# Performance work log

Hardware: AMD Instinct MI355X
Metric: run time of the kernel (lower is better)

The kernel has to match this reference:

```python
import jax, jax.numpy as jnp
import numpy as np

HEADS = 8

def setup_inputs() -> dict:
    key = jax.random.key(0)
    ks = jax.random.split(key, 6)
    N, C, L = 8, 512, 2048
    s = 0.02
    return {
        'x':  jax.random.normal(ks[0], (N, C, L), dtype=jnp.float32),
        'Wq': jax.random.normal(ks[1], (C, C), dtype=jnp.float32) * s,
        'Wk': jax.random.normal(ks[2], (C, C), dtype=jnp.float32) * s,
        'Wv': jax.random.normal(ks[3], (C, C), dtype=jnp.float32) * s,
        'Wo': jax.random.normal(ks[4], (C, C), dtype=jnp.float32) * s,
        'bo': jnp.zeros((C,), dtype=jnp.float32),
    }

def reference(x, Wq, Wk, Wv, Wo, bo):
    N, C, L = x.shape
    h = HEADS
    d = C // h
    scale = C ** (-0.5)  # note: scales by full channels, as in the original

    def proj(W):
        # Conv1d(k=1, bias=False) == per-position linear: [N,C,L] -> [N,L,h,d]
        y = jnp.einsum('oc,ncl->nlo', W, x)
        return y.reshape(N, L, h, d)

    q, k, v = proj(Wq), proj(Wk), proj(Wv)

    qk = jnp.einsum('nqhd,nkhd->nhqk', q, k)  # [N,h,L,L]
    causal_mask = jnp.tril(jnp.ones((L, L), dtype=bool))
    qk = jnp.where(causal_mask, qk, -jnp.inf)
    attn = jax.nn.softmax(qk * scale, axis=-1)

    out = jnp.einsum('nhqk,nkhd->nqhd', attn, v)  # [N,L,h,d]
    out = out.reshape(N, L, C).transpose(0, 2, 1)  # n (h d) l
    return jnp.einsum('oc,ncl->nol', Wo, out) + bo[None, :, None]
```

## Files before the change

### kernel.cpp

```cpp
#include <hip/hip_runtime.h>
#include <math.h>

typedef __bf16 bf16;
typedef __attribute__((ext_vector_type(8))) __bf16 bf16x8;
typedef __attribute__((ext_vector_type(4))) float f32x4;
typedef unsigned short u16;
typedef unsigned int u32;

constexpr int Nn = 8, Cc = 512, Ll = 2048, Hh = 8, Dd = 64;
constexpr float kScale = 0.044194173824159216f;
constexpr float kQexp2 = kScale * 1.44269504088896341f;
constexpr size_t NCL = (size_t)Nn * Cc * Ll;
constexpr size_t WSZ = (size_t)Cc * Cc;

static __device__ __forceinline__ u16 bfbits(bf16 v) {
    union { bf16 b; u16 u; } x; x.b = v; return x.u;
}
static __device__ __forceinline__ u32 fbits(float f) {
    union { float f; u32 u; } x; x.f = f; return x.u;
}
static __device__ __forceinline__ float fexp2(float x) {
#if __has_builtin(__builtin_amdgcn_exp2f)
    return __builtin_amdgcn_exp2f(x);
#else
    return exp2f(x);
#endif
}

#define MFMA(a, b, c) __builtin_amdgcn_mfma_f32_16x16x32_bf16((a), (b), (c), 0, 0, 0)

static __device__ __forceinline__ void async16(const bf16* g, bf16* l) {
    __builtin_amdgcn_global_load_lds(
        (const __attribute__((address_space(1))) void*)g,
        (__attribute__((address_space(3))) void*)l, 16, 0, 0);
}

__global__ __launch_bounds__(256) void xpose_kernel(
    const float* __restrict__ x, bf16* __restrict__ xT)
{
    __shared__ bf16 Ts[64][72];
    const int lt = blockIdx.x, ct = blockIdx.y, n = blockIdx.z;
    const int tid = threadIdx.x;

    const int cr = tid >> 2, l0 = (tid & 3) * 16;
    const float* src = x + ((size_t)(n * Cc + ct * 64 + cr)) * Ll + lt * 64 + l0;
#pragma unroll
    for (int i = 0; i < 4; i++) {
        float4 v = *(const float4*)(src + i * 4);
        Ts[l0 + i * 4 + 0][cr] = (bf16)v.x;
        Ts[l0 + i * 4 + 1][cr] = (bf16)v.y;
        Ts[l0 + i * 4 + 2][cr] = (bf16)v.z;
        Ts[l0 + i * 4 + 3][cr] = (bf16)v.w;
    }
    __syncthreads();

    const int lr = tid >> 2, c0 = (tid & 3) * 16;
    bf16* dst = xT + ((size_t)(n * Ll + lt * 64 + lr)) * Cc + ct * 64 + c0;
    *(bf16x8*)(dst)     = *(const bf16x8*)&Ts[lr][c0];
    *(bf16x8*)(dst + 8) = *(const bf16x8*)&Ts[lr][c0 + 8];
}

__global__ __launch_bounds__(256) void cvtw_kernel(
    const float* __restrict__ Wq, const float* __restrict__ Wk,
    const float* __restrict__ Wv, const float* __restrict__ Wo,
    bf16* __restrict__ Wb)
{
    size_t i = (size_t)blockIdx.x * 256 + threadIdx.x;
    int w = (int)(i >> 16);
    size_t o = i & 65535;
    const float* src = (w == 0) ? Wq : (w == 1) ? Wk : (w == 2) ? Wv : Wo;
    float4 v = ((const float4*)src)[o];
    ushort4 u;
    u.x = bfbits((bf16)v.x); u.y = bfbits((bf16)v.y);
    u.z = bfbits((bf16)v.z); u.w = bfbits((bf16)v.w);
    *(ushort4*)(Wb + (size_t)w * WSZ + o * 4) = u;
}

__global__ __launch_bounds__(256) void qkv_gemm(
    const bf16* __restrict__ xT, const bf16* __restrict__ Wb,
    bf16* __restrict__ Qt, bf16* __restrict__ Kt, bf16* __restrict__ Vb)
{
    const int lt = blockIdx.x, ow = blockIdx.y, n = blockIdx.z;
    const int widx = ow >> 2, otile = ow & 3;

    __shared__ bf16 Xs[128 * 64];
    __shared__ bf16 Ws[128 * 64];

    const int tid = threadIdx.x;
    const int lane = tid & 63, wv = tid >> 6;
    const int m = lane & 15, quad = lane >> 4;
    const int rh = wv & 1, ch = wv >> 1;

    const bf16* __restrict__ W = Wb + (size_t)widx * WSZ + (size_t)otile * 128 * Cc;
    const bf16* __restrict__ X = xT + (size_t)(n * Ll + lt * 128) * Cc;

    int srow[4], scol[4];
#pragma unroll
    for (int i = 0; i < 4; i++) {
        int q = i * 256 + tid;
        srow[i] = q >> 3;
        scol[i] = ((q ^ (q >> 3)) & 7) * 8;
    }

    f32x4 acc[4][4] = {};

    for (int c0 = 0; c0 < Cc; c0 += 64) {
#pragma unroll
        for (int i = 0; i < 4; i++)
            async16(&X[(size_t)srow[i] * Cc + c0 + scol[i]], &Xs[(i * 256 + tid) * 8]);
#pragma unroll
        for (int i = 0; i < 4; i++)
            async16(&W[(size_t)srow[i] * Cc + c0 + scol[i]], &Ws[(i * 256 + tid) * 8]);
        __syncthreads();

        const bf16* TA = (widx < 2) ? Xs : Ws;
        const bf16* TB = (widx < 2) ? Ws : Xs;
#pragma unroll
        for (int kk = 0; kk < 2; kk++) {
            const int sw = (((kk * 4 + quad) ^ (m & 7)) * 8);
            bf16x8 af[4], bfr[4];
#pragma unroll
            for (int t = 0; t < 4; t++)
                af[t] = *(const bf16x8*)&TA[(rh * 64 + t * 16 + m) * 64 + sw];
#pragma unroll
            for (int u = 0; u < 4; u++)
                bfr[u] = *(const bf16x8*)&TB[(ch * 64 + u * 16 + m) * 64 + sw];
#pragma unroll
            for (int t = 0; t < 4; t++)
#pragma unroll
                for (int u = 0; u < 4; u++)
                    acc[t][u] = MFMA(af[t], bfr[u], acc[t][u]);
        }
        __syncthreads();
    }

    if (widx < 2) {
        const float fq = (widx == 0) ? kQexp2 : 1.0f;
        bf16* __restrict__ OUT = (widx == 0) ? Qt : Kt;
#pragma unroll
        for (int u = 0; u < 4; u++) {
            const int o = otile * 128 + ch * 64 + u * 16 + m;
            const int h = o >> 6, d = o & 63;
            bf16* base = OUT + (size_t)(n * Hh + h) * Ll * Dd + d;
#pragma unroll
            for (int t = 0; t < 4; t++) {
                const int l0 = lt * 128 + rh * 64 + t * 16 + quad * 4;
#pragma unroll
                for (int r = 0; r < 4; r++)
                    base[(size_t)(l0 + r) * Dd] = (bf16)(acc[t][u][r] * fq);
            }
        }
    } else {
#pragma unroll
        for (int t = 0; t < 4; t++) {
            const int ob = otile * 128 + rh * 64 + t * 16 + quad * 4;
#pragma unroll
            for (int r = 0; r < 4; r++) {
                const int oo = ob + r, h = oo >> 6, d = oo & 63;
                bf16* base = Vb + ((size_t)(n * Hh + h) * Dd + d) * Ll;
#pragma unroll
                for (int u = 0; u < 4; u++)
                    base[lt * 128 + ch * 64 + u * 16 + m] = (bf16)acc[t][u][r];
            }
        }
    }
}

__global__ __launch_bounds__(256, 3) void attn_mfma(
    const bf16* __restrict__ Qt, const bf16* __restrict__ Kt,
    const bf16* __restrict__ Vb, bf16* __restrict__ AO)
{
    const int jp = blockIdx.x;
    const int h  = blockIdx.y, n = blockIdx.z;

    __shared__ bf16 KV[2][2][64 * 72];
    __shared__ bf16 Pbuf[4][16 * 72];

    const int tid = threadIdx.x;
    const int lane = tid & 63, wv = tid >> 6;
    const int m = lane & 15, quad = lane >> 4;

    const size_t bnh = (size_t)(n * Hh + h) * Ll * Dd;
    const bf16* __restrict__ Qh = Qt + bnh;
    const bf16* __restrict__ Kh = Kt + bnh;
    const bf16* __restrict__ Vh = Vb + bnh;

    const int srow = tid >> 3;
    const int sc8  = (tid & 7) * 8;

    bf16* const Pw = &Pbuf[wv][0];

    bf16x8 ones;
#pragma unroll
    for (int j = 0; j < 8; j++) ones[j] = (bf16)1.0f;

    int koff[4];
#pragma unroll
    for (int r = 0; r < 4; r++) koff[r] = quad * 4 + r - m;

#pragma unroll 1
    for (int ph = 0; ph < 2; ph++) {
        const int st = ph ? (15 - jp) : jp;
        const int R  = st * 128;
        const int nk = 2 * st + 2;
        const int qrow0 = R + wv * 32;

        bf16x8 qf[2][2];
#pragma unroll
        for (int rt = 0; rt < 2; rt++)
#pragma unroll
            for (int hf = 0; hf < 2; hf++)
                qf[rt][hf] = *(const bf16x8*)&Qh[(size_t)(qrow0 + rt * 16 + m) * Dd + hf * 32 + quad * 8];

        f32x4 O[2][4] = {};
        f32x4 Ls[2] = {};

        {
            bf16x8 ka  = *(const bf16x8*)&Kh[(size_t)(srow) * Dd + sc8];
            bf16x8 kb2 = *(const bf16x8*)&Kh[(size_t)(srow + 32) * Dd + sc8];
            bf16x8 va  = *(const bf16x8*)&Vh[(size_t)(srow) * Ll + sc8];
            bf16x8 vb2 = *(const bf16x8*)&Vh[(size_t)(srow + 32) * Ll + sc8];
            *(bf16x8*)&KV[0][0][srow * 72 + sc8] = ka;
            *(bf16x8*)&KV[0][0][(srow + 32) * 72 + sc8] = kb2;
            *(bf16x8*)&KV[0][1][srow * 72 + sc8] = va;
            *(bf16x8*)&KV[0][1][(srow + 32) * 72 + sc8] = vb2;
        }
        __syncthreads();

        for (int kt = 0; kt < nk; kt++) {
            const int cur = kt & 1, nxt = cur ^ 1;
            const int kb = kt * 64;
            const bool do_pf = (kt + 1 < nk);

            bf16x8 ka, kb2, va, vb2;
            if (do_pf) {
                const int kn = kb + 64;
                ka  = *(const bf16x8*)&Kh[(size_t)(kn + srow) * Dd + sc8];
                kb2 = *(const bf16x8*)&Kh[(size_t)(kn + srow + 32) * Dd + sc8];
                va  = *(const bf16x8*)&Vh[(size_t)(srow) * Ll + kn + sc8];
                vb2 = *(const bf16x8*)&Vh[(size_t)(srow + 32) * Ll + kn + sc8];
            }

            const bf16* Ks = &KV[cur][0][0];
            const bf16* Vs = &KV[cur][1][0];

            f32x4 St[2][4] = {};
#pragma unroll
            for (int t = 0; t < 4; t++) {
                bf16x8 kf0 = *(const bf16x8*)&Ks[(t * 16 + m) * 72 + quad * 8];
                bf16x8 kf1 = *(const bf16x8*)&Ks[(t * 16 + m) * 72 + 32 + quad * 8];
                St[0][t] = MFMA(kf0, qf[0][0], St[0][t]);
                St[0][t] = MFMA(kf1, qf[0][1], St[0][t]);
                St[1][t] = MFMA(kf0, qf[1][0], St[1][t]);
                St[1][t] = MFMA(kf1, qf[1][1], St[1][t]);
            }

            const bool skip0 = (kb > qrow0 + 15);
            const bool skip1 = (kb > qrow0 + 16 + 15);

#pragma unroll
            for (int rt = 0; rt < 2; rt++) {
                if (rt == 0 ? skip0 : skip1) continue;
                const int qtb = qrow0 + rt * 16;
                const bool dg = (kb + 63 > qtb);
                const int thr = qtb - kb;

#pragma unroll
                for (int t = 0; t < 4; t++) {
                    float p0 = fexp2(St[rt][t][0]);
                    float p1 = fexp2(St[rt][t][1]);
                    float p2 = fexp2(St[rt][t][2]);
                    float p3 = fexp2(St[rt][t][3]);
                    if (dg) {
                        if (t * 16 + koff[0] > thr) p0 = 0.f;
                        if (t * 16 + koff[1] > thr) p1 = 0.f;
                        if (t * 16 + koff[2] > thr) p2 = 0.f;
                        if (t * 16 + koff[3] > thr) p3 = 0.f;
                    }
                    u32 pk0 = (fbits(p0) >> 16) | (fbits(p1) & 0xFFFF0000u);
                    u32 pk1 = (fbits(p2) >> 16) | (fbits(p3) & 0xFFFF0000u);
                    *(uint2*)&Pw[m * 72 + t * 16 + quad * 4] = make_uint2(pk0, pk1);
                }
                asm volatile("s_waitcnt lgkmcnt(0)" ::: "memory");

                bf16x8 pf0 = *(const bf16x8*)&Pw[m * 72 + quad * 8];
                bf16x8 pf1 = *(const bf16x8*)&Pw[m * 72 + 32 + quad * 8];

                Ls[rt] = MFMA(pf0, ones, Ls[rt]);
                Ls[rt] = MFMA(pf1, ones, Ls[rt]);
#pragma unroll
                for (int t = 0; t < 4; t++) {
                    bf16x8 vf0 = *(const bf16x8*)&Vs[(t * 16 + m) * 72 + quad * 8];
                    bf16x8 vf1 = *(const bf16x8*)&Vs[(t * 16 + m) * 72 + 32 + quad * 8];
                    O[rt][t] = MFMA(pf0, vf0, O[rt][t]);
                    O[rt][t] = MFMA(pf1, vf1, O[rt][t]);
                }
            }

            __syncthreads();
            if (do_pf) {
                *(bf16x8*)&KV[nxt][0][srow * 72 + sc8] = ka;
                *(bf16x8*)&KV[nxt][0][(srow + 32) * 72 + sc8] = kb2;
                *(bf16x8*)&KV[nxt][1][srow * 72 + sc8] = va;
                *(bf16x8*)&KV[nxt][1][(srow + 32) * 72 + sc8] = vb2;
                __syncthreads();
            }
        }

        const size_t aobase = (size_t)n * Ll * Cc + (size_t)h * 64;
#pragma unroll
        for (int rt = 0; rt < 2; rt++) {
            f32x4 inv;
#pragma unroll
            for (int r = 0; r < 4; r++) inv[r] = 1.0f / Ls[rt][r];
#pragma unroll
            for (int t = 0; t < 4; t++)
#pragma unroll
                for (int r = 0; r < 4; r++) {
                    const int q = qrow0 + rt * 16 + quad * 4 + r;
                    AO[aobase + (size_t)q * Cc + t * 16 + m] =
                        (bf16)(O[rt][t][r] * inv[r]);
                }
        }
    }
}

__global__ __launch_bounds__(256) void out_gemm(
    const bf16* __restrict__ AO, const bf16* __restrict__ Wb,
    const float* __restrict__ bo, float* __restrict__ out)
{
    const int lt = blockIdx.x, ot = blockIdx.y, n = blockIdx.z;

    __shared__ bf16 Ws[128 * 64];
    __shared__ bf16 Bs[128 * 64];

    const int tid = threadIdx.x;
    const int lane = tid & 63, wv = tid >> 6;
    const int m = lane & 15, quad = lane >> 4;
    const int rh = wv & 1, ch = wv >> 1;

    const bf16* __restrict__ W = Wb + 3 * WSZ + (size_t)ot * 128 * Cc;
    const bf16* __restrict__ B = AO + (size_t)(n * Ll + lt * 128) * Cc;

    int srow[4], scol[4];
#pragma unroll
    for (int i = 0; i < 4; i++) {
        int q = i * 256 + tid;
        srow[i] = q >> 3;
        scol[i] = ((q ^ (q >> 3)) & 7) * 8;
    }

    f32x4 acc[4][4] = {};

    for (int c0 = 0; c0 < Cc; c0 += 64) {
#pragma unroll
        for (int i = 0; i < 4; i++)
            async16(&W[(size_t)srow[i] * Cc + c0 + scol[i]], &Ws[(i * 256 + tid) * 8]);
#pragma unroll
        for (int i = 0; i < 4; i++)
            async16(&B[(size_t)srow[i] * Cc + c0 + scol[i]], &Bs[(i * 256 + tid) * 8]);
        __syncthreads();

#pragma unroll
        for (int kk = 0; kk < 2; kk++) {
            const int sw = (((kk * 4 + quad) ^ (m & 7)) * 8);
            bf16x8 af[4], bfr[4];
#pragma unroll
            for (int t = 0; t < 4; t++)
                af[t] = *(const bf16x8*)&Ws[(rh * 64 + t * 16 + m) * 64 + sw];
#pragma unroll
            for (int u = 0; u < 4; u++)
                bfr[u] = *(const bf16x8*)&Bs[(ch * 64 + u * 16 + m) * 64 + sw];
#pragma unroll
            for (int t = 0; t < 4; t++)
#pragma unroll
                for (int u = 0; u < 4; u++)
                    acc[t][u] = MFMA(af[t], bfr[u], acc[t][u]);
        }
        __syncthreads();
    }

#pragma unroll
    for (int t = 0; t < 4; t++) {
        const int ob = ot * 128 + rh * 64 + t * 16 + quad * 4;
#pragma unroll
        for (int r = 0; r < 4; r++) {
            const int o = ob + r;
            const float b = bo[o];
            float* base = out + ((size_t)n * Cc + o) * Ll + lt * 128 + ch * 64;
#pragma unroll
            for (int u = 0; u < 4; u++)
                base[u * 16 + m] = acc[t][u][r] + b;
        }
    }
}

extern "C" void kernel_launch(void* const* d_in, const int* in_sizes, int n_in,
                              void* d_out, int out_size, void* d_ws, size_t ws_size,
                              hipStream_t stream)
{
    const float* x  = (const float*)d_in[0];
    const float* Wq = (const float*)d_in[1];
    const float* Wk = (const float*)d_in[2];
    const float* Wv = (const float*)d_in[3];
    const float* Wo = (const float*)d_in[4];
    const float* bo = (const float*)d_in[5];
    float* out = (float*)d_out;

    bf16* ws = (bf16*)d_ws;
    bf16* xT = ws;
    bf16* Wb = xT + NCL;
    bf16* Qt = Wb + 4 * WSZ;
    bf16* Kt = Qt + NCL;
    bf16* Vb = Kt + NCL;
    bf16* AO = Vb + NCL;

    xpose_kernel<<<dim3(32, 8, Nn), 256, 0, stream>>>(x, xT);
    cvtw_kernel<<<1024, 256, 0, stream>>>(Wq, Wk, Wv, Wo, Wb);
    qkv_gemm<<<dim3(16, 12, Nn), 256, 0, stream>>>(xT, Wb, Qt, Kt, Vb);
    attn_mfma<<<dim3(8, Hh, Nn), 256, 0, stream>>>(Qt, Kt, Vb, AO);
    out_gemm<<<dim3(16, 4, Nn), 256, 0, stream>>>(AO, Wb, bo, out);
}
```

Baseline: 219.9 us.

## Use 512-thread attention blocks with one 16-row query tile per wave

Attention blocks grow from 4 to 8 waves. Each wave now owns a single 16-row query tile instead of two, and each thread stages one K row and one V row instead of two. The grid is reordered so the head index varies fastest, which groups blocks of the same query stripe. The aim is more waves in flight to hide latency, plus finer per-wave causal skipping. In exchange, each K/V tile in shared memory is reused across fewer query rows per wave, and barriers now span more waves. A barrier is also added after each phase.

```diff
diff --git a/kernel.cpp b/kernel.cpp
--- a/kernel.cpp
+++ b/kernel.cpp
@@ -166,15 +166,16 @@
     }
 }
 
-__global__ __launch_bounds__(256, 3) void attn_mfma(
+__global__ __launch_bounds__(512, 4) void attn_mfma(
     const bf16* __restrict__ Qt, const bf16* __restrict__ Kt,
     const bf16* __restrict__ Vb, bf16* __restrict__ AO)
 {
-    const int jp = blockIdx.x;
-    const int h  = blockIdx.y, n = blockIdx.z;
+    const int h  = blockIdx.x;
+    const int jp = blockIdx.y;
+    const int n  = blockIdx.z;
 
     __shared__ bf16 KV[2][2][64 * 72];
-    __shared__ bf16 Pbuf[4][16 * 72];
+    __shared__ bf16 Pbuf[8][16 * 72];
 
     const int tid = threadIdx.x;
     const int lane = tid & 63, wv = tid >> 6;
@@ -203,27 +204,19 @@
         const int st = ph ? (15 - jp) : jp;
         const int R  = st * 128;
         const int nk = 2 * st + 2;
-        const int qrow0 = R + wv * 32;
-
-        bf16x8 qf[2][2];
-#pragma unroll
-        for (int rt = 0; rt < 2; rt++)
-#pragma unroll
-            for (int hf = 0; hf < 2; hf++)
-                qf[rt][hf] = *(const bf16x8*)&Qh[(size_t)(qrow0 + rt * 16 + m) * Dd + hf * 32 + quad * 8];
-
-        f32x4 O[2][4] = {};
-        f32x4 Ls[2] = {};
+        const int qrow0 = R + wv * 16;
+
+        bf16x8 qf0 = *(const bf16x8*)&Qh[(size_t)(qrow0 + m) * Dd + quad * 8];
+        bf16x8 qf1 = *(const bf16x8*)&Qh[(size_t)(qrow0 + m) * Dd + 32 + quad * 8];
+
+        f32x4 O[4] = {};
+        f32x4 Ls = {};
 
         {
-            bf16x8 ka  = *(const bf16x8*)&Kh[(size_t)(srow) * Dd + sc8];
-            bf16x8 kb2 = *(const bf16x8*)&Kh[(size_t)(srow + 32) * Dd + sc8];
-            bf16x8 va  = *(const bf16x8*)&Vh[(size_t)(srow) * Ll + sc8];
-            bf16x8 vb2 = *(const bf16x8*)&Vh[(size_t)(srow + 32) * Ll + sc8];
+            bf16x8 ka = *(const bf16x8*)&Kh[(size_t)srow * Dd + sc8];
+            bf16x8 va = *(const bf16x8*)&Vh[(size_t)srow * Ll + sc8];
             *(bf16x8*)&KV[0][0][srow * 72 + sc8] = ka;
-            *(bf16x8*)&KV[0][0][(srow + 32) * 72 + sc8] = kb2;
             *(bf16x8*)&KV[0][1][srow * 72 + sc8] = va;
-            *(bf16x8*)&KV[0][1][(srow + 32) * 72 + sc8] = vb2;
         }
         __syncthreads();
 
@@ -232,45 +225,35 @@
             const int kb = kt * 64;
             const bool do_pf = (kt + 1 < nk);
 
-            bf16x8 ka, kb2, va, vb2;
+            bf16x8 ka, va;
             if (do_pf) {
                 const int kn = kb + 64;
-                ka  = *(const bf16x8*)&Kh[(size_t)(kn + srow) * Dd + sc8];
-                kb2 = *(const bf16x8*)&Kh[(size_t)(kn + srow + 32) * Dd + sc8];
-                va  = *(const bf16x8*)&Vh[(size_t)(srow) * Ll + kn + sc8];
-                vb2 = *(const bf16x8*)&Vh[(size_t)(srow + 32) * Ll + kn + sc8];
-            }
-
-            const bf16* Ks = &KV[cur][0][0];
-            const bf16* Vs = &KV[cur][1][0];
-
-            f32x4 St[2][4] = {};
-#pragma unroll
-            for (int t = 0; t < 4; t++) {
-                bf16x8 kf0 = *(const bf16x8*)&Ks[(t * 16 + m) * 72 + quad * 8];
-                bf16x8 kf1 = *(const bf16x8*)&Ks[(t * 16 + m) * 72 + 32 + quad * 8];
-                St[0][t] = MFMA(kf0, qf[0][0], St[0][t]);
-                St[0][t] = MFMA(kf1, qf[0][1], St[0][t]);
-                St[1][t] = MFMA(kf0, qf[1][0], St[1][t]);
-                St[1][t] = MFMA(kf1, qf[1][1], St[1][t]);
-            }
-
-            const bool skip0 = (kb > qrow0 + 15);
-            const bool skip1 = (kb > qrow0 + 16 + 15);
-
-#pragma unroll
-            for (int rt = 0; rt < 2; rt++) {
-                if (rt == 0 ? skip0 : skip1) continue;
-                const int qtb = qrow0 + rt * 16;
-                const bool dg = (kb + 63 > qtb);
-                const int thr = qtb - kb;
-
+                ka = *(const bf16x8*)&Kh[(size_t)(kn + srow) * Dd + sc8];
+                va = *(const bf16x8*)&Vh[(size_t)srow * Ll + kn + sc8];
+            }
+
+            const bool skip = (kb > qrow0 + 15);
+            if (!skip) {
+                const bf16* Ks = &KV[cur][0][0];
+                const bf16* Vs = &KV[cur][1][0];
+
+                f32x4 St[4] = {};
 #pragma unroll
                 for (int t = 0; t < 4; t++) {
-                    float p0 = fexp2(St[rt][t][0]);
-                    float p1 = fexp2(St[rt][t][1]);
-                    float p2 = fexp2(St[rt][t][2]);
-                    float p3 = fexp2(St[rt][t][3]);
+                    bf16x8 kf0 = *(const bf16x8*)&Ks[(t * 16 + m) * 72 + quad * 8];
+                    bf16x8 kf1 = *(const bf16x8*)&Ks[(t * 16 + m) * 72 + 32 + quad * 8];
+                    St[t] = MFMA(kf0, qf0, St[t]);
+                    St[t] = MFMA(kf1, qf1, St[t]);
+                }
+
+                const bool dg = (kb + 63 > qrow0);
+                const int thr = qrow0 - kb;
+#pragma unroll
+                for (int t = 0; t < 4; t++) {
+                    float p0 = fexp2(St[t][0]);
+                    float p1 = fexp2(St[t][1]);
+                    float p2 = fexp2(St[t][2]);
+                    float p3 = fexp2(St[t][3]);
                     if (dg) {
                         if (t * 16 + koff[0] > thr) p0 = 0.f;
                         if (t * 16 + koff[1] > thr) p1 = 0.f;
@@ -286,42 +269,38 @@
                 bf16x8 pf0 = *(const bf16x8*)&Pw[m * 72 + quad * 8];
                 bf16x8 pf1 = *(const bf16x8*)&Pw[m * 72 + 32 + quad * 8];
 
-                Ls[rt] = MFMA(pf0, ones, Ls[rt]);
-                Ls[rt] = MFMA(pf1, ones, Ls[rt]);
+                Ls = MFMA(pf0, ones, Ls);
+                Ls = MFMA(pf1, ones, Ls);
 #pragma unroll
                 for (int t = 0; t < 4; t++) {
                     bf16x8 vf0 = *(const bf16x8*)&Vs[(t * 16 + m) * 72 + quad * 8];
                     bf16x8 vf1 = *(const bf16x8*)&Vs[(t * 16 + m) * 72 + 32 + quad * 8];
-                    O[rt][t] = MFMA(pf0, vf0, O[rt][t]);
-                    O[rt][t] = MFMA(pf1, vf1, O[rt][t]);
+                    O[t] = MFMA(pf0, vf0, O[t]);
+                    O[t] = MFMA(pf1, vf1, O[t]);
                 }
             }
 
             __syncthreads();
             if (do_pf) {
                 *(bf16x8*)&KV[nxt][0][srow * 72 + sc8] = ka;
-                *(bf16x8*)&KV[nxt][0][(srow + 32) * 72 + sc8] = kb2;
                 *(bf16x8*)&KV[nxt][1][srow * 72 + sc8] = va;
-                *(bf16x8*)&KV[nxt][1][(srow + 32) * 72 + sc8] = vb2;
                 __syncthreads();
             }
         }
 
+        f32x4 inv;
+#pragma unroll
+        for (int r = 0; r < 4; r++) inv[r] = 1.0f / Ls[r];
+
         const size_t aobase = (size_t)n * Ll * Cc + (size_t)h * 64;
 #pragma unroll
-        for (int rt = 0; rt < 2; rt++) {
-            f32x4 inv;
-#pragma unroll
-            for (int r = 0; r < 4; r++) inv[r] = 1.0f / Ls[rt][r];
-#pragma unroll
-            for (int t = 0; t < 4; t++)
-#pragma unroll
-                for (int r = 0; r < 4; r++) {
-                    const int q = qrow0 + rt * 16 + quad * 4 + r;
-                    AO[aobase + (size_t)q * Cc + t * 16 + m] =
-                        (bf16)(O[rt][t][r] * inv[r]);
-                }
-        }
+        for (int t = 0; t < 4; t++)
+#pragma unroll
+            for (int r = 0; r < 4; r++) {
+                const int q = qrow0 + quad * 4 + r;
+                AO[aobase + (size_t)q * Cc + t * 16 + m] = (bf16)(O[t][r] * inv[r]);
+            }
+        __syncthreads();
     }
 }
 
@@ -418,6 +397,6 @@
     xpose_kernel<<<dim3(32, 8, Nn), 256, 0, stream>>>(x, xT);
     cvtw_kernel<<<1024, 256, 0, stream>>>(Wq, Wk, Wv, Wo, Wb);
     qkv_gemm<<<dim3(16, 12, Nn), 256, 0, stream>>>(xT, Wb, Qt, Kt, Vb);
-    attn_mfma<<<dim3(8, Hh, Nn), 256, 0, stream>>>(Qt, Kt, Vb, AO);
+    attn_mfma<<<dim3(Hh, 8, Nn), 512, 0, stream>>>(Qt, Kt, Vb, AO);
     out_gemm<<<dim3(16, 4, Nn), 256, 0, stream>>>(AO, Wb, bo, out);
 }
```

After: 204.2 us. -7.2%, faster.
